# Kernel tuning notes

Measured on AMD Instinct MI355X. Metric: run time of the kernel, lower is better.

The kernel has to match this reference:

```python
import jax, jax.numpy as jnp
import numpy as np

D_MODEL = 768
NUM_HEADS = 12
D_K = D_MODEL // NUM_HEADS
BATCH = 1
SEQ = 4096


def setup_inputs() -> dict:
    key = jax.random.key(0)
    ks = jax.random.split(key, 11)
    s = 0.02
    inp = {
        'Q': jax.random.normal(ks[0], (BATCH, SEQ, D_MODEL), jnp.float32),
        'K': jax.random.normal(ks[1], (BATCH, SEQ, D_MODEL), jnp.float32),
        'V': jax.random.normal(ks[2], (BATCH, SEQ, D_MODEL), jnp.float32),
        'Wq': jax.random.normal(ks[3], (D_MODEL, D_MODEL), jnp.float32) * s,
        'bq': jnp.zeros((D_MODEL,), jnp.float32),
        'Wk': jax.random.normal(ks[4], (D_MODEL, D_MODEL), jnp.float32) * s,
        'bk': jnp.zeros((D_MODEL,), jnp.float32),
        'Wv': jax.random.normal(ks[5], (D_MODEL, D_MODEL), jnp.float32) * s,
        'bv': jnp.zeros((D_MODEL,), jnp.float32),
        'Wo': jax.random.normal(ks[6], (D_MODEL, D_MODEL), jnp.float32) * s,
        'bo': jnp.zeros((D_MODEL,), jnp.float32),
    }
    return inp


def reference(Q, K, V, Wq, bq, Wk, bk, Wv, bv, Wo, bo):
    B, S, _ = Q.shape
    # Linear projections (torch Linear: x @ W^T + b)
    q = Q @ Wq.T + bq
    k = K @ Wk.T + bk
    v = V @ Wv.T + bv
    # split heads: (B, S, D) -> (B, H, S, d_k)
    def split(x):
        return x.reshape(B, S, NUM_HEADS, D_K).transpose(0, 2, 1, 3)
    q, k, v = split(q), split(k), split(v)
    # scaled dot-product attention (dropout = identity in eval)
    scores = jnp.einsum('bhqd,bhkd->bhqk', q, k) / jnp.sqrt(jnp.float32(D_K))
    attn_weights = jax.nn.softmax(scores, axis=-1)
    ctx = jnp.einsum('bhqk,bhkd->bhqd', attn_weights, v)
    # merge heads and output projection
    ctx = ctx.transpose(0, 2, 1, 3).reshape(B, S, D_MODEL)
    output = ctx @ Wo.T + bo
    return (output, attn_weights)
```

## Files before the change

kernel.cpp:

```cpp
#include <hip/hip_runtime.h>
#include <hip/hip_bf16.h>

#define S 4096
#define DM 768
#define NH 12
#define DK 64
#define KSPLIT 2
#define KHALF (S / KSPLIT)
#define RPARTS 8
#define RCHUNK (S / RPARTS)

typedef __bf16 bf16x8 __attribute__((ext_vector_type(8)));
typedef __bf16 bf16x4 __attribute__((ext_vector_type(4)));
typedef float f32x4 __attribute__((ext_vector_type(4)));
using bf16 = __hip_bfloat16;

__device__ inline bf16x8 load_frag(const bf16* p) {
    return *reinterpret_cast<const bf16x8*>(p);
}

__global__ void k_detect(const unsigned int* __restrict__ q, int* __restrict__ flag) {
    const int lane = threadIdx.x;
    int cnt = 0;
    for (int i = lane; i < 1024; i += 64) {
        const unsigned int w = q[i];
        const int e = (w >> 7) & 0xFF;
        if (e >= 192 || (e > 0 && e < 64)) cnt++;
    }
    for (int m = 1; m < 64; m <<= 1) cnt += __shfl_xor(cnt, m, 64);
    if (lane == 0) flag[0] = (cnt > 64) ? 1 : 0;
}

__device__ inline void cast_body(const void* src, bf16* dst, int n, int isf32) {
    const int stride = gridDim.x * 256 * 8;
    for (int i = (blockIdx.x * 256 + threadIdx.x) * 8; i < n; i += stride) {
        if (isf32) {
            const float* s = (const float*)src + i;
            float4 a = *(const float4*)(s);
            float4 b = *(const float4*)(s + 4);
            bf16x8 o;
            o[0] = (__bf16)a.x; o[1] = (__bf16)a.y; o[2] = (__bf16)a.z; o[3] = (__bf16)a.w;
            o[4] = (__bf16)b.x; o[5] = (__bf16)b.y; o[6] = (__bf16)b.z; o[7] = (__bf16)b.w;
            *reinterpret_cast<bf16x8*>(dst + i) = o;
        } else {
            *reinterpret_cast<bf16x8*>(dst + i) =
                *reinterpret_cast<const bf16x8*>((const __bf16*)src + i);
        }
    }
}

__global__ __launch_bounds__(256) void k_cast3(
    const void* s0, const void* s1, const void* s2,
    bf16* d0, bf16* d1, bf16* d2, int n, const int* __restrict__ flag) {
    const int t = blockIdx.y;
    const void* s = (t == 0) ? s0 : (t == 1) ? s1 : s2;
    bf16* d = (t == 0) ? d0 : (t == 1) ? d1 : d2;
    cast_body(s, d, n, flag[0]);
}

__global__ __launch_bounds__(256) void k_cast4(
    const void* s0, const void* s1, const void* s2, const void* s3,
    bf16* d0, bf16* d1, bf16* d2, bf16* d3, int n, const int* __restrict__ flag) {
    const int t = blockIdx.y;
    const void* s = (t == 0) ? s0 : (t == 1) ? s1 : (t == 2) ? s2 : s3;
    bf16* d = (t == 0) ? d0 : (t == 1) ? d1 : (t == 2) ? d2 : d3;
    cast_body(s, d, n, flag[0]);
}

__device__ inline void proj_body(
    const bf16* __restrict__ X, const bf16* __restrict__ W,
    const bf16* __restrict__ bias, void* __restrict__ dstv, int mode, int isf32)
{
    const int lane = threadIdx.x & 63;
    const int w    = threadIdx.x >> 6;
    const int lr   = lane & 15, lg = lane >> 4;
    const int rbase = blockIdx.x * 64 + w * 16;
    const int nbase = blockIdx.y * 64;

    f32x4 acc[4] = {};
    const bf16* xrow = X + (size_t)(rbase + lr) * DM + lg * 8;
    for (int kk = 0; kk < DM; kk += 32) {
        bf16x8 a = load_frag(xrow + kk);
#pragma unroll
        for (int nt = 0; nt < 4; ++nt) {
            bf16x8 b = load_frag(W + (size_t)(nbase + nt * 16 + lr) * DM + kk + lg * 8);
            acc[nt] = __builtin_amdgcn_mfma_f32_16x16x32_bf16(a, b, acc[nt], 0, 0, 0);
        }
    }
#pragma unroll
    for (int nt = 0; nt < 4; ++nt) {
        const int col = nbase + nt * 16 + lr;
        const float bv = __bfloat162float(bias[col]);
#pragma unroll
        for (int r = 0; r < 4; ++r) {
            const int row = rbase + lg * 4 + r;
            const float v = acc[nt][r] + bv;
            size_t off;
            if (mode == 2) off = (size_t)col * S + row;
            else           off = (size_t)(col >> 6) * (S * DK) + (size_t)row * DK + (col & 63);
            ((bf16*)dstv)[off] = __float2bfloat16(v);
        }
    }
}

__global__ __launch_bounds__(256) void k_proj_qkv(
    const bf16* __restrict__ Qc, const bf16* __restrict__ Kc, const bf16* __restrict__ Vc,
    const bf16* __restrict__ Wq, const bf16* __restrict__ Wk, const bf16* __restrict__ Wv,
    const bf16* __restrict__ bq, const bf16* __restrict__ bk, const bf16* __restrict__ bv,
    bf16* __restrict__ qh, bf16* __restrict__ kh, bf16* __restrict__ vt,
    const int* __restrict__ flag)
{
    const int z = blockIdx.z;
    const bf16* X = (z == 0) ? Qc : (z == 1) ? Kc : Vc;
    const bf16* W = (z == 0) ? Wq : (z == 1) ? Wk : Wv;
    const bf16* B = (z == 0) ? bq : (z == 1) ? bk : bv;
    bf16* D      = (z == 0) ? qh : (z == 1) ? kh : vt;
    proj_body(X, W, B, D, (z == 2) ? 2 : 0, flag[0]);
}

__global__ __launch_bounds__(256) void k_proj_out(
    const bf16* __restrict__ ctxp, const bf16* __restrict__ W,
    const bf16* __restrict__ bias, void* __restrict__ dstv,
    const int* __restrict__ flag)
{
    const int isf32 = flag[0];
    const int lane = threadIdx.x & 63;
    const int w    = threadIdx.x >> 6;
    const int lr   = lane & 15, lg = lane >> 4;
    const int rbase = blockIdx.x * 64 + w * 16;
    const int nbase = blockIdx.y * 64;

    f32x4 acc[4] = {};
    const bf16* x0 = ctxp + (size_t)(rbase + lr) * DM + lg * 8;
    const bf16* x1 = x0 + (size_t)S * DM;
    for (int kk = 0; kk < DM; kk += 32) {
        bf16x8 a0 = load_frag(x0 + kk);
        bf16x8 a1 = load_frag(x1 + kk);
        bf16x8 a;
#pragma unroll
        for (int j = 0; j < 8; ++j)
            a[j] = (__bf16)((float)a0[j] + (float)a1[j]);
#pragma unroll
        for (int nt = 0; nt < 4; ++nt) {
            bf16x8 b = load_frag(W + (size_t)(nbase + nt * 16 + lr) * DM + kk + lg * 8);
            acc[nt] = __builtin_amdgcn_mfma_f32_16x16x32_bf16(a, b, acc[nt], 0, 0, 0);
        }
    }
#pragma unroll
    for (int nt = 0; nt < 4; ++nt) {
        const int col = nbase + nt * 16 + lr;
        const float bv = __bfloat162float(bias[col]);
#pragma unroll
        for (int r = 0; r < 4; ++r) {
            const int row = rbase + lg * 4 + r;
            const float v = acc[nt][r] + bv;
            const size_t off = (size_t)row * DM + col;
            if (isf32) ((float*)dstv)[off] = v;
            else       ((bf16*)dstv)[off] = __float2bfloat16(v);
        }
    }
}

__global__ __launch_bounds__(256) void k_rowsum(
    const bf16* __restrict__ qh, const bf16* __restrict__ kh,
    float* __restrict__ rs)
{
    const int lane = threadIdx.x & 63;
    const int w    = threadIdx.x >> 6;
    const int lr   = lane & 15;
    const int lg   = lane >> 4;
    const int h    = blockIdx.y;
    const int part = blockIdx.z;
    const int qw   = blockIdx.x * 256 + w * 64;

    const bf16* qb = qh + (size_t)h * (S * DK);
    const bf16* kb = kh + (size_t)h * (S * DK);
    bf16x8 aq[4][2];
#pragma unroll
    for (int qs = 0; qs < 4; ++qs) {
        aq[qs][0] = load_frag(qb + (size_t)(qw + qs * 16 + lr) * DK + lg * 8);
        aq[qs][1] = load_frag(qb + (size_t)(qw + qs * 16 + lr) * DK + 32 + lg * 8);
    }

    float s[4] = {0.f, 0.f, 0.f, 0.f};
    for (int kp = part * RCHUNK; kp < part * RCHUNK + RCHUNK; kp += 16) {
        bf16x8 b0 = load_frag(kb + (size_t)(kp + lr) * DK + lg * 8);
        bf16x8 b1 = load_frag(kb + (size_t)(kp + lr) * DK + 32 + lg * 8);
#pragma unroll
        for (int qs = 0; qs < 4; ++qs) {
            f32x4 d = {};
            d = __builtin_amdgcn_mfma_f32_16x16x32_bf16(b0, aq[qs][0], d, 0, 0, 0);
            d = __builtin_amdgcn_mfma_f32_16x16x32_bf16(b1, aq[qs][1], d, 0, 0, 0);
            s[qs] += __expf(d[0] * 0.125f) + __expf(d[1] * 0.125f) +
                     __expf(d[2] * 0.125f) + __expf(d[3] * 0.125f);
        }
    }
#pragma unroll
    for (int qs = 0; qs < 4; ++qs) {
        float v = s[qs];
        v += __shfl_xor(v, 16, 64);
        v += __shfl_xor(v, 32, 64);
        if (lg == 0)
            rs[((size_t)part * NH + h) * S + qw + qs * 16 + lr] = v;
    }
}

__global__ __launch_bounds__(256) void k_attn(
    const bf16* __restrict__ qh, const bf16* __restrict__ kh,
    const bf16* __restrict__ vt, const float* __restrict__ rs,
    void* __restrict__ doutv, bf16* __restrict__ ctxp,
    const int* __restrict__ flag)
{
    __shared__ __align__(16) bf16 Plds[4][2][16][136];
    const int isf32 = flag[0];
    const int lane = threadIdx.x & 63;
    const int w    = threadIdx.x >> 6;
    const int lr   = lane & 15, lg = lane >> 4;
    const int h    = blockIdx.y;
    const int half = blockIdx.z;
    const int q0w  = blockIdx.x * 128 + w * 32;
    const int k0   = half * KHALF;

    const bf16* qb = qh + (size_t)h * (S * DK);
    const bf16* kb = kh + (size_t)h * (S * DK);
    const bf16* vb = vt + (size_t)h * (S * DK);

    bf16x8 aq[2][2];
    float  inv[2];
#pragma unroll
    for (int qs = 0; qs < 2; ++qs) {
        const int qr = q0w + qs * 16 + lr;
        aq[qs][0] = load_frag(qb + (size_t)qr * DK + lg * 8);
        aq[qs][1] = load_frag(qb + (size_t)qr * DK + 32 + lg * 8);
        float ssum = 0.f;
#pragma unroll
        for (int p = 0; p < RPARTS; ++p)
            ssum += rs[((size_t)p * NH + h) * S + qr];
        inv[qs] = 1.0f / ssum;
    }

    float* poutF = (float*)doutv + (size_t)S * DM + (size_t)h * S * S;
    bf16*  poutB = (bf16*)doutv  + (size_t)S * DM + (size_t)h * S * S;

    const int fr2 = lane >> 5;
    const int fc2 = (lane & 31) * 4;

    f32x4 acc[2][4] = {};
    for (int tp = 0; tp < KHALF / 128; ++tp) {
#pragma unroll
        for (int tt = 0; tt < 2; ++tt) {
            const int kt = k0 + tp * 128 + tt * 64;
            const int cb = tt * 64;
            bf16x8 vv[4][2];
#pragma unroll
            for (int dt = 0; dt < 4; ++dt) {
                vv[dt][0] = load_frag(vb + (size_t)(dt * 16 + lr) * S + kt + lg * 8);
                vv[dt][1] = load_frag(vb + (size_t)(dt * 16 + lr) * S + kt + 32 + lg * 8);
            }
#pragma unroll
            for (int sub = 0; sub < 4; ++sub) {
                const int kp = kt + sub * 16;
                bf16x8 b0 = load_frag(kb + (size_t)(kp + lr) * DK + lg * 8);
                bf16x8 b1 = load_frag(kb + (size_t)(kp + lr) * DK + 32 + lg * 8);
#pragma unroll
                for (int qs = 0; qs < 2; ++qs) {
                    f32x4 d = {};
                    d = __builtin_amdgcn_mfma_f32_16x16x32_bf16(b0, aq[qs][0], d, 0, 0, 0);
                    d = __builtin_amdgcn_mfma_f32_16x16x32_bf16(b1, aq[qs][1], d, 0, 0, 0);
                    bf16x4 pv;
                    pv[0] = (__bf16)(__expf(d[0] * 0.125f) * inv[qs]);
                    pv[1] = (__bf16)(__expf(d[1] * 0.125f) * inv[qs]);
                    pv[2] = (__bf16)(__expf(d[2] * 0.125f) * inv[qs]);
                    pv[3] = (__bf16)(__expf(d[3] * 0.125f) * inv[qs]);
                    *reinterpret_cast<bf16x4*>(
                        &Plds[w][qs][lr][cb + sub * 16 + 4 * lg]) = pv;
                }
            }
            bf16x8 ap[2][2];
#pragma unroll
            for (int qs = 0; qs < 2; ++qs) {
                ap[qs][0] = *reinterpret_cast<const bf16x8*>(&Plds[w][qs][lr][cb + lg * 8]);
                ap[qs][1] = *reinterpret_cast<const bf16x8*>(&Plds[w][qs][lr][cb + 32 + lg * 8]);
            }
#pragma unroll
            for (int dt = 0; dt < 4; ++dt) {
#pragma unroll
                for (int qs = 0; qs < 2; ++qs) {
                    acc[qs][dt] = __builtin_amdgcn_mfma_f32_16x16x32_bf16(ap[qs][0], vv[dt][0], acc[qs][dt], 0, 0, 0);
                    acc[qs][dt] = __builtin_amdgcn_mfma_f32_16x16x32_bf16(ap[qs][1], vv[dt][1], acc[qs][dt], 0, 0, 0);
                }
            }
        }
        const int ktbase = k0 + tp * 128;
        if (isf32) {
#pragma unroll
            for (int j = 0; j < 16; ++j) {
                const int row = 2 * j + fr2;
                const int qs = row >> 4, rr = row & 15;
                bf16x4 x = *reinterpret_cast<const bf16x4*>(&Plds[w][qs][rr][fc2]);
                f32x4 o;
                o[0] = (float)x[0]; o[1] = (float)x[1];
                o[2] = (float)x[2]; o[3] = (float)x[3];
                __builtin_nontemporal_store(
                    o, reinterpret_cast<f32x4*>(
                           poutF + (size_t)(q0w + row) * S + ktbase + fc2));
            }
        } else {
#pragma unroll
            for (int j = 0; j < 16; ++j) {
                const int row = 2 * j + fr2;
                const int qs = row >> 4, rr = row & 15;
                bf16x4 x = *reinterpret_cast<const bf16x4*>(&Plds[w][qs][rr][fc2]);
                *reinterpret_cast<bf16x4*>(
                    poutB + (size_t)(q0w + row) * S + ktbase + fc2) = x;
            }
        }
    }
    bf16* cp = ctxp + (size_t)half * S * DM;
#pragma unroll
    for (int qs = 0; qs < 2; ++qs)
#pragma unroll
        for (int dt = 0; dt < 4; ++dt)
#pragma unroll
            for (int r = 0; r < 4; ++r)
                cp[(size_t)(q0w + qs * 16 + 4 * lg + r) * DM + h * DK + dt * 16 + lr] =
                    __float2bfloat16(acc[qs][dt][r]);
}

extern "C" void kernel_launch(void* const* d_in, const int* in_sizes, int n_in,
                              void* d_out, int out_size, void* d_ws, size_t ws_size,
                              hipStream_t stream) {
    char* wsb = (char*)d_ws;
    int*   flag = (int*)wsb;
    float* rs   = (float*)(wsb + 16);
    bf16*  conv = (bf16*)(wsb + 16 + (size_t)RPARTS * NH * S * 4);

    const size_t nQ = (size_t)S * DM, nW = (size_t)DM * DM, nB = DM;
    bf16* Qc  = conv;
    bf16* Kc  = Qc + nQ;
    bf16* Vc  = Kc + nQ;
    bf16* Wqc = Vc + nQ;
    bf16* Wkc = Wqc + nW;
    bf16* Wvc = Wkc + nW;
    bf16* Woc = Wvc + nW;
    bf16* bqc = Woc + nW;
    bf16* bkc = bqc + nB;
    bf16* bvc = bkc + nB;
    bf16* boc = bvc + nB;
    bf16* qh  = boc + nB;
    bf16* kh  = qh + nQ;
    bf16* vt  = kh + nQ;
    bf16* ctxp = Qc;

    const size_t need = (size_t)((char*)(vt + nQ) - wsb);
    if (ws_size < need) return;

    dim3 blk(256);
    k_detect<<<1, 64, 0, stream>>>((const unsigned int*)d_in[0], flag);

    k_cast3<<<dim3((int)(nQ / 2048), 3), blk, 0, stream>>>(
        d_in[0], d_in[1], d_in[2], Qc, Kc, Vc, (int)nQ, flag);
    k_cast4<<<dim3((int)(nW / 2048), 4), blk, 0, stream>>>(
        d_in[3], d_in[5], d_in[7], d_in[9], Wqc, Wkc, Wvc, Woc, (int)nW, flag);
    k_cast4<<<dim3(1, 4), blk, 0, stream>>>(
        d_in[4], d_in[6], d_in[8], d_in[10], bqc, bkc, bvc, boc, (int)nB, flag);

    k_proj_qkv<<<dim3(S / 64, DM / 64, 3), blk, 0, stream>>>(
        Qc, Kc, Vc, Wqc, Wkc, Wvc, bqc, bkc, bvc, qh, kh, vt, flag);
    k_rowsum<<<dim3(S / 256, NH, RPARTS), blk, 0, stream>>>(qh, kh, rs);
    k_attn<<<dim3(S / 128, NH, KSPLIT), blk, 0, stream>>>(qh, kh, vt, rs, d_out, ctxp, flag);
    k_proj_out<<<dim3(S / 64, DM / 64), blk, 0, stream>>>(ctxp, Woc, boc, d_out, flag);
}
```

Baseline: 470.4 us.

## Double-buffer K/V register tiles in attention kernel and fold normalization into exp

The attention kernel now prefetches the next 64-key K and V fragments into a second register set while the current tile's QK^T, softmax and PV MFMAs run, so global load latency overlaps with compute. The softmax normalization becomes exp(x*0.125 - log(sum)) through a single FMA instead of a multiply after the exp. Launch bounds now request 2 blocks per CU. The extra register buffers raise register pressure and the occupancy hint may cause spills. On the last iteration the prefetch reloads the same tile, which is redundant but harmless.

Measured after the change: 468.5 us. No clear change (-0.4%).

```diff
diff --git a/kernel.cpp b/kernel.cpp
--- a/kernel.cpp
+++ b/kernel.cpp
@@ -205,7 +205,59 @@
     }
 }
 
-__global__ __launch_bounds__(256) void k_attn(
+__device__ inline void load_ktile(const bf16* kb, int kt, int lr, int lg,
+                                  bf16x8 dst[4][2]) {
+#pragma unroll
+    for (int sub = 0; sub < 4; ++sub) {
+        dst[sub][0] = load_frag(kb + (size_t)(kt + sub * 16 + lr) * DK + lg * 8);
+        dst[sub][1] = load_frag(kb + (size_t)(kt + sub * 16 + lr) * DK + 32 + lg * 8);
+    }
+}
+__device__ inline void load_vtile(const bf16* vb, int kt, int lr, int lg,
+                                  bf16x8 dst[4][2]) {
+#pragma unroll
+    for (int dt = 0; dt < 4; ++dt) {
+        dst[dt][0] = load_frag(vb + (size_t)(dt * 16 + lr) * S + kt + lg * 8);
+        dst[dt][1] = load_frag(vb + (size_t)(dt * 16 + lr) * S + kt + 32 + lg * 8);
+    }
+}
+__device__ inline void qk_tile(const bf16x8 kc[4][2], const bf16x8 aq[2][2],
+                               const float linv[2], bf16 Pw[2][16][136],
+                               int cb, int lr, int lg) {
+#pragma unroll
+    for (int sub = 0; sub < 4; ++sub) {
+#pragma unroll
+        for (int qs = 0; qs < 2; ++qs) {
+            f32x4 d = {};
+            d = __builtin_amdgcn_mfma_f32_16x16x32_bf16(kc[sub][0], aq[qs][0], d, 0, 0, 0);
+            d = __builtin_amdgcn_mfma_f32_16x16x32_bf16(kc[sub][1], aq[qs][1], d, 0, 0, 0);
+            bf16x4 pv;
+            pv[0] = (__bf16)__expf(__builtin_fmaf(d[0], 0.125f, linv[qs]));
+            pv[1] = (__bf16)__expf(__builtin_fmaf(d[1], 0.125f, linv[qs]));
+            pv[2] = (__bf16)__expf(__builtin_fmaf(d[2], 0.125f, linv[qs]));
+            pv[3] = (__bf16)__expf(__builtin_fmaf(d[3], 0.125f, linv[qs]));
+            *reinterpret_cast<bf16x4*>(&Pw[qs][lr][cb + sub * 16 + 4 * lg]) = pv;
+        }
+    }
+}
+__device__ inline void pv_tile(const bf16x8 vc[4][2], const bf16 Pw[2][16][136],
+                               f32x4 acc[2][4], int cb, int lr, int lg) {
+    bf16x8 ap[2][2];
+#pragma unroll
+    for (int qs = 0; qs < 2; ++qs) {
+        ap[qs][0] = *reinterpret_cast<const bf16x8*>(&Pw[qs][lr][cb + lg * 8]);
+        ap[qs][1] = *reinterpret_cast<const bf16x8*>(&Pw[qs][lr][cb + 32 + lg * 8]);
+    }
+#pragma unroll
+    for (int dt = 0; dt < 4; ++dt)
+#pragma unroll
+        for (int qs = 0; qs < 2; ++qs) {
+            acc[qs][dt] = __builtin_amdgcn_mfma_f32_16x16x32_bf16(ap[qs][0], vc[dt][0], acc[qs][dt], 0, 0, 0);
+            acc[qs][dt] = __builtin_amdgcn_mfma_f32_16x16x32_bf16(ap[qs][1], vc[dt][1], acc[qs][dt], 0, 0, 0);
+        }
+}
+
+__global__ __launch_bounds__(256, 2) void k_attn(
     const bf16* __restrict__ qh, const bf16* __restrict__ kh,
     const bf16* __restrict__ vt, const float* __restrict__ rs,
     void* __restrict__ doutv, bf16* __restrict__ ctxp,
@@ -220,13 +272,14 @@
     const int half = blockIdx.z;
     const int q0w  = blockIdx.x * 128 + w * 32;
     const int k0   = half * KHALF;
+    const int NT   = KHALF / 64;
 
     const bf16* qb = qh + (size_t)h * (S * DK);
     const bf16* kb = kh + (size_t)h * (S * DK);
     const bf16* vb = vt + (size_t)h * (S * DK);
 
     bf16x8 aq[2][2];
-    float  inv[2];
+    float  linv[2];
 #pragma unroll
     for (int qs = 0; qs < 2; ++qs) {
         const int qr = q0w + qs * 16 + lr;
@@ -236,62 +289,31 @@
 #pragma unroll
         for (int p = 0; p < RPARTS; ++p)
             ssum += rs[((size_t)p * NH + h) * S + qr];
-        inv[qs] = 1.0f / ssum;
+        linv[qs] = -__logf(ssum);
     }
 
     float* poutF = (float*)doutv + (size_t)S * DM + (size_t)h * S * S;
     bf16*  poutB = (bf16*)doutv  + (size_t)S * DM + (size_t)h * S * S;
-
     const int fr2 = lane >> 5;
     const int fc2 = (lane & 31) * 4;
 
+    bf16x8 kA[4][2], vA[4][2], kB[4][2], vB[4][2];
+    load_ktile(kb, k0, lr, lg, kA);
+    load_vtile(vb, k0, lr, lg, vA);
+
     f32x4 acc[2][4] = {};
-    for (int tp = 0; tp < KHALF / 128; ++tp) {
-#pragma unroll
-        for (int tt = 0; tt < 2; ++tt) {
-            const int kt = k0 + tp * 128 + tt * 64;
-            const int cb = tt * 64;
-            bf16x8 vv[4][2];
-#pragma unroll
-            for (int dt = 0; dt < 4; ++dt) {
-                vv[dt][0] = load_frag(vb + (size_t)(dt * 16 + lr) * S + kt + lg * 8);
-                vv[dt][1] = load_frag(vb + (size_t)(dt * 16 + lr) * S + kt + 32 + lg * 8);
-            }
-#pragma unroll
-            for (int sub = 0; sub < 4; ++sub) {
-                const int kp = kt + sub * 16;
-                bf16x8 b0 = load_frag(kb + (size_t)(kp + lr) * DK + lg * 8);
-                bf16x8 b1 = load_frag(kb + (size_t)(kp + lr) * DK + 32 + lg * 8);
-#pragma unroll
-                for (int qs = 0; qs < 2; ++qs) {
-                    f32x4 d = {};
-                    d = __builtin_amdgcn_mfma_f32_16x16x32_bf16(b0, aq[qs][0], d, 0, 0, 0);
-                    d = __builtin_amdgcn_mfma_f32_16x16x32_bf16(b1, aq[qs][1], d, 0, 0, 0);
-                    bf16x4 pv;
-                    pv[0] = (__bf16)(__expf(d[0] * 0.125f) * inv[qs]);
-                    pv[1] = (__bf16)(__expf(d[1] * 0.125f) * inv[qs]);
-                    pv[2] = (__bf16)(__expf(d[2] * 0.125f) * inv[qs]);
-                    pv[3] = (__bf16)(__expf(d[3] * 0.125f) * inv[qs]);
-                    *reinterpret_cast<bf16x4*>(
-                        &Plds[w][qs][lr][cb + sub * 16 + 4 * lg]) = pv;
-                }
-            }
-            bf16x8 ap[2][2];
-#pragma unroll
-            for (int qs = 0; qs < 2; ++qs) {
-                ap[qs][0] = *reinterpret_cast<const bf16x8*>(&Plds[w][qs][lr][cb + lg * 8]);
-                ap[qs][1] = *reinterpret_cast<const bf16x8*>(&Plds[w][qs][lr][cb + 32 + lg * 8]);
-            }
-#pragma unroll
-            for (int dt = 0; dt < 4; ++dt) {
-#pragma unroll
-                for (int qs = 0; qs < 2; ++qs) {
-                    acc[qs][dt] = __builtin_amdgcn_mfma_f32_16x16x32_bf16(ap[qs][0], vv[dt][0], acc[qs][dt], 0, 0, 0);
-                    acc[qs][dt] = __builtin_amdgcn_mfma_f32_16x16x32_bf16(ap[qs][1], vv[dt][1], acc[qs][dt], 0, 0, 0);
-                }
-            }
-        }
-        const int ktbase = k0 + tp * 128;
+    for (int p = 0; p < NT / 2; ++p) {
+        const int ktA  = k0 + 2 * p * 64;
+        const int ktB  = ktA + 64;
+        const int ktA2 = (2 * p + 2 < NT) ? ktB + 64 : ktB;
+        load_ktile(kb, ktB, lr, lg, kB);
+        load_vtile(vb, ktB, lr, lg, vB);
+        qk_tile(kA, aq, linv, Plds[w], 0, lr, lg);
+        pv_tile(vA, Plds[w], acc, 0, lr, lg);
+        load_ktile(kb, ktA2, lr, lg, kA);
+        load_vtile(vb, ktA2, lr, lg, vA);
+        qk_tile(kB, aq, linv, Plds[w], 64, lr, lg);
+        pv_tile(vB, Plds[w], acc, 64, lr, lg);
         if (isf32) {
 #pragma unroll
             for (int j = 0; j < 16; ++j) {
@@ -303,7 +325,7 @@
                 o[2] = (float)x[2]; o[3] = (float)x[3];
                 __builtin_nontemporal_store(
                     o, reinterpret_cast<f32x4*>(
-                           poutF + (size_t)(q0w + row) * S + ktbase + fc2));
+                           poutF + (size_t)(q0w + row) * S + ktA + fc2));
             }
         } else {
 #pragma unroll
@@ -312,7 +334,7 @@
                 const int qs = row >> 4, rr = row & 15;
                 bf16x4 x = *reinterpret_cast<const bf16x4*>(&Plds[w][qs][rr][fc2]);
                 *reinterpret_cast<bf16x4*>(
-                    poutB + (size_t)(q0w + row) * S + ktbase + fc2) = x;
+                    poutB + (size_t)(q0w + row) * S + ktA + fc2) = x;
             }
         }
     }
```

## Drop key split in attention, merge cast kernels, fold normalization into exp

Applied to the files above, without the earlier changes.

The attention kernel no longer splits the key range in two. Each 128-thread block now covers 64 queries over all keys in 256-key groups, so the output projection reads a single context buffer instead of summing two partials. The three cast launches are merged into one kernel driven by an argument struct. The softmax normalization is folded into the exponent as an added log term, which removes a multiply. The cost is fewer, longer-running attention blocks (the same 768 blocks but half as many waves), which may lower latency hiding.

New measurement: 464.7 us. Within noise of the previous version (-1.2%).

```diff
diff --git a/kernel.cpp b/kernel.cpp
--- a/kernel.cpp
+++ b/kernel.cpp
@@ -5,8 +5,6 @@
 #define DM 768
 #define NH 12
 #define DK 64
-#define KSPLIT 2
-#define KHALF (S / KSPLIT)
 #define RPARTS 8
 #define RCHUNK (S / RPARTS)
 
@@ -31,40 +29,33 @@
     if (lane == 0) flag[0] = (cnt > 64) ? 1 : 0;
 }
 
-__device__ inline void cast_body(const void* src, bf16* dst, int n, int isf32) {
+struct CastArgs {
+    const void* s[11];
+    bf16* d[11];
+    int n[11];
+};
+
+__global__ __launch_bounds__(256) void k_cast_all(CastArgs a, const int* __restrict__ flag) {
+    const int t = blockIdx.y;
+    const void* src = a.s[t];
+    bf16* dst = a.d[t];
+    const int n = a.n[t];
+    const int isf32 = flag[0];
     const int stride = gridDim.x * 256 * 8;
     for (int i = (blockIdx.x * 256 + threadIdx.x) * 8; i < n; i += stride) {
         if (isf32) {
             const float* s = (const float*)src + i;
-            float4 a = *(const float4*)(s);
-            float4 b = *(const float4*)(s + 4);
+            float4 x = *(const float4*)(s);
+            float4 y = *(const float4*)(s + 4);
             bf16x8 o;
-            o[0] = (__bf16)a.x; o[1] = (__bf16)a.y; o[2] = (__bf16)a.z; o[3] = (__bf16)a.w;
-            o[4] = (__bf16)b.x; o[5] = (__bf16)b.y; o[6] = (__bf16)b.z; o[7] = (__bf16)b.w;
+            o[0] = (__bf16)x.x; o[1] = (__bf16)x.y; o[2] = (__bf16)x.z; o[3] = (__bf16)x.w;
+            o[4] = (__bf16)y.x; o[5] = (__bf16)y.y; o[6] = (__bf16)y.z; o[7] = (__bf16)y.w;
             *reinterpret_cast<bf16x8*>(dst + i) = o;
         } else {
             *reinterpret_cast<bf16x8*>(dst + i) =
                 *reinterpret_cast<const bf16x8*>((const __bf16*)src + i);
         }
     }
-}
-
-__global__ __launch_bounds__(256) void k_cast3(
-    const void* s0, const void* s1, const void* s2,
-    bf16* d0, bf16* d1, bf16* d2, int n, const int* __restrict__ flag) {
-    const int t = blockIdx.y;
-    const void* s = (t == 0) ? s0 : (t == 1) ? s1 : s2;
-    bf16* d = (t == 0) ? d0 : (t == 1) ? d1 : d2;
-    cast_body(s, d, n, flag[0]);
-}
-
-__global__ __launch_bounds__(256) void k_cast4(
-    const void* s0, const void* s1, const void* s2, const void* s3,
-    bf16* d0, bf16* d1, bf16* d2, bf16* d3, int n, const int* __restrict__ flag) {
-    const int t = blockIdx.y;
-    const void* s = (t == 0) ? s0 : (t == 1) ? s1 : (t == 2) ? s2 : s3;
-    bf16* d = (t == 0) ? d0 : (t == 1) ? d1 : (t == 2) ? d2 : d3;
-    cast_body(s, d, n, flag[0]);
 }
 
 __device__ inline void proj_body(
@@ -119,7 +110,7 @@
 }
 
 __global__ __launch_bounds__(256) void k_proj_out(
-    const bf16* __restrict__ ctxp, const bf16* __restrict__ W,
+    const bf16* __restrict__ ctx, const bf16* __restrict__ W,
     const bf16* __restrict__ bias, void* __restrict__ dstv,
     const int* __restrict__ flag)
 {
@@ -131,15 +122,9 @@
     const int nbase = blockIdx.y * 64;
 
     f32x4 acc[4] = {};
-    const bf16* x0 = ctxp + (size_t)(rbase + lr) * DM + lg * 8;
-    const bf16* x1 = x0 + (size_t)S * DM;
+    const bf16* xrow = ctx + (size_t)(rbase + lr) * DM + lg * 8;
     for (int kk = 0; kk < DM; kk += 32) {
-        bf16x8 a0 = load_frag(x0 + kk);
-        bf16x8 a1 = load_frag(x1 + kk);
-        bf16x8 a;
-#pragma unroll
-        for (int j = 0; j < 8; ++j)
-            a[j] = (__bf16)((float)a0[j] + (float)a1[j]);
+        bf16x8 a = load_frag(xrow + kk);
 #pragma unroll
         for (int nt = 0; nt < 4; ++nt) {
             bf16x8 b = load_frag(W + (size_t)(nbase + nt * 16 + lr) * DM + kk + lg * 8);
@@ -205,28 +190,26 @@
     }
 }
 
-__global__ __launch_bounds__(256) void k_attn(
+__global__ __launch_bounds__(128) void k_attn(
     const bf16* __restrict__ qh, const bf16* __restrict__ kh,
     const bf16* __restrict__ vt, const float* __restrict__ rs,
-    void* __restrict__ doutv, bf16* __restrict__ ctxp,
+    void* __restrict__ doutv, bf16* __restrict__ ctx,
     const int* __restrict__ flag)
 {
-    __shared__ __align__(16) bf16 Plds[4][2][16][136];
+    __shared__ __align__(16) bf16 Plds[2][2][16][264];
     const int isf32 = flag[0];
     const int lane = threadIdx.x & 63;
     const int w    = threadIdx.x >> 6;
     const int lr   = lane & 15, lg = lane >> 4;
     const int h    = blockIdx.y;
-    const int half = blockIdx.z;
-    const int q0w  = blockIdx.x * 128 + w * 32;
-    const int k0   = half * KHALF;
+    const int q0w  = blockIdx.x * 64 + w * 32;
 
     const bf16* qb = qh + (size_t)h * (S * DK);
     const bf16* kb = kh + (size_t)h * (S * DK);
     const bf16* vb = vt + (size_t)h * (S * DK);
 
     bf16x8 aq[2][2];
-    float  inv[2];
+    float  linv[2];
 #pragma unroll
     for (int qs = 0; qs < 2; ++qs) {
         const int qr = q0w + qs * 16 + lr;
@@ -236,20 +219,17 @@
 #pragma unroll
         for (int p = 0; p < RPARTS; ++p)
             ssum += rs[((size_t)p * NH + h) * S + qr];
-        inv[qs] = 1.0f / ssum;
+        linv[qs] = -__logf(ssum);
     }
 
     float* poutF = (float*)doutv + (size_t)S * DM + (size_t)h * S * S;
     bf16*  poutB = (bf16*)doutv  + (size_t)S * DM + (size_t)h * S * S;
 
-    const int fr2 = lane >> 5;
-    const int fc2 = (lane & 31) * 4;
-
     f32x4 acc[2][4] = {};
-    for (int tp = 0; tp < KHALF / 128; ++tp) {
-#pragma unroll
-        for (int tt = 0; tt < 2; ++tt) {
-            const int kt = k0 + tp * 128 + tt * 64;
+    for (int g = 0; g < S / 256; ++g) {
+#pragma unroll
+        for (int tt = 0; tt < 4; ++tt) {
+            const int kt = g * 256 + tt * 64;
             const int cb = tt * 64;
             bf16x8 vv[4][2];
 #pragma unroll
@@ -268,10 +248,10 @@
                     d = __builtin_amdgcn_mfma_f32_16x16x32_bf16(b0, aq[qs][0], d, 0, 0, 0);
                     d = __builtin_amdgcn_mfma_f32_16x16x32_bf16(b1, aq[qs][1], d, 0, 0, 0);
                     bf16x4 pv;
-                    pv[0] = (__bf16)(__expf(d[0] * 0.125f) * inv[qs]);
-                    pv[1] = (__bf16)(__expf(d[1] * 0.125f) * inv[qs]);
-                    pv[2] = (__bf16)(__expf(d[2] * 0.125f) * inv[qs]);
-                    pv[3] = (__bf16)(__expf(d[3] * 0.125f) * inv[qs]);
+                    pv[0] = (__bf16)__expf(__builtin_fmaf(d[0], 0.125f, linv[qs]));
+                    pv[1] = (__bf16)__expf(__builtin_fmaf(d[1], 0.125f, linv[qs]));
+                    pv[2] = (__bf16)__expf(__builtin_fmaf(d[2], 0.125f, linv[qs]));
+                    pv[3] = (__bf16)__expf(__builtin_fmaf(d[3], 0.125f, linv[qs]));
                     *reinterpret_cast<bf16x4*>(
                         &Plds[w][qs][lr][cb + sub * 16 + 4 * lg]) = pv;
                 }
@@ -291,39 +271,36 @@
                 }
             }
         }
-        const int ktbase = k0 + tp * 128;
+        const int ktbase = g * 256;
         if (isf32) {
 #pragma unroll
-            for (int j = 0; j < 16; ++j) {
-                const int row = 2 * j + fr2;
-                const int qs = row >> 4, rr = row & 15;
-                bf16x4 x = *reinterpret_cast<const bf16x4*>(&Plds[w][qs][rr][fc2]);
+            for (int j = 0; j < 32; ++j) {
+                const int qs = j >> 4, rr = j & 15;
+                bf16x4 x = *reinterpret_cast<const bf16x4*>(&Plds[w][qs][rr][lane * 4]);
                 f32x4 o;
                 o[0] = (float)x[0]; o[1] = (float)x[1];
                 o[2] = (float)x[2]; o[3] = (float)x[3];
                 __builtin_nontemporal_store(
                     o, reinterpret_cast<f32x4*>(
-                           poutF + (size_t)(q0w + row) * S + ktbase + fc2));
+                           poutF + (size_t)(q0w + j) * S + ktbase + lane * 4));
             }
         } else {
 #pragma unroll
-            for (int j = 0; j < 16; ++j) {
-                const int row = 2 * j + fr2;
-                const int qs = row >> 4, rr = row & 15;
-                bf16x4 x = *reinterpret_cast<const bf16x4*>(&Plds[w][qs][rr][fc2]);
+            for (int j = 0; j < 32; ++j) {
+                const int qs = j >> 4, rr = j & 15;
+                bf16x4 x = *reinterpret_cast<const bf16x4*>(&Plds[w][qs][rr][lane * 4]);
                 *reinterpret_cast<bf16x4*>(
-                    poutB + (size_t)(q0w + row) * S + ktbase + fc2) = x;
-            }
-        }
-    }
-    bf16* cp = ctxp + (size_t)half * S * DM;
+                    poutB + (size_t)(q0w + j) * S + ktbase + lane * 4) = x;
+            }
+        }
+    }
 #pragma unroll
     for (int qs = 0; qs < 2; ++qs)
 #pragma unroll
         for (int dt = 0; dt < 4; ++dt)
 #pragma unroll
             for (int r = 0; r < 4; ++r)
-                cp[(size_t)(q0w + qs * 16 + 4 * lg + r) * DM + h * DK + dt * 16 + lr] =
+                ctx[(size_t)(q0w + qs * 16 + 4 * lg + r) * DM + h * DK + dt * 16 + lr] =
                     __float2bfloat16(acc[qs][dt][r]);
 }
 
@@ -350,7 +327,7 @@
     bf16* qh  = boc + nB;
     bf16* kh  = qh + nQ;
     bf16* vt  = kh + nQ;
-    bf16* ctxp = Qc;
+    bf16* ctx = Qc;
 
     const size_t need = (size_t)((char*)(vt + nQ) - wsb);
     if (ws_size < need) return;
@@ -358,16 +335,23 @@
     dim3 blk(256);
     k_detect<<<1, 64, 0, stream>>>((const unsigned int*)d_in[0], flag);
 
-    k_cast3<<<dim3((int)(nQ / 2048), 3), blk, 0, stream>>>(
-        d_in[0], d_in[1], d_in[2], Qc, Kc, Vc, (int)nQ, flag);
-    k_cast4<<<dim3((int)(nW / 2048), 4), blk, 0, stream>>>(
-        d_in[3], d_in[5], d_in[7], d_in[9], Wqc, Wkc, Wvc, Woc, (int)nW, flag);
-    k_cast4<<<dim3(1, 4), blk, 0, stream>>>(
-        d_in[4], d_in[6], d_in[8], d_in[10], bqc, bkc, bvc, boc, (int)nB, flag);
+    CastArgs ca;
+    ca.s[0] = d_in[0];  ca.d[0] = Qc;   ca.n[0] = (int)nQ;
+    ca.s[1] = d_in[1];  ca.d[1] = Kc;   ca.n[1] = (int)nQ;
+    ca.s[2] = d_in[2];  ca.d[2] = Vc;   ca.n[2] = (int)nQ;
+    ca.s[3] = d_in[3];  ca.d[3] = Wqc;  ca.n[3] = (int)nW;
+    ca.s[4] = d_in[5];  ca.d[4] = Wkc;  ca.n[4] = (int)nW;
+    ca.s[5] = d_in[7];  ca.d[5] = Wvc;  ca.n[5] = (int)nW;
+    ca.s[6] = d_in[9];  ca.d[6] = Woc;  ca.n[6] = (int)nW;
+    ca.s[7] = d_in[4];  ca.d[7] = bqc;  ca.n[7] = (int)nB;
+    ca.s[8] = d_in[6];  ca.d[8] = bkc;  ca.n[8] = (int)nB;
+    ca.s[9] = d_in[8];  ca.d[9] = bvc;  ca.n[9] = (int)nB;
+    ca.s[10] = d_in[10]; ca.d[10] = boc; ca.n[10] = (int)nB;
+    k_cast_all<<<dim3(512, 11), blk, 0, stream>>>(ca, flag);
 
     k_proj_qkv<<<dim3(S / 64, DM / 64, 3), blk, 0, stream>>>(
         Qc, Kc, Vc, Wqc, Wkc, Wvc, bqc, bkc, bvc, qh, kh, vt, flag);
     k_rowsum<<<dim3(S / 256, NH, RPARTS), blk, 0, stream>>>(qh, kh, rs);
-    k_attn<<<dim3(S / 128, NH, KSPLIT), blk, 0, stream>>>(qh, kh, vt, rs, d_out, ctxp, flag);
-    k_proj_out<<<dim3(S / 64, DM / 64), blk, 0, stream>>>(ctxp, Woc, boc, d_out, flag);
-}
+    k_attn<<<dim3(S / 64, NH), dim3(128), 0, stream>>>(qh, kh, vt, rs, d_out, ctx, flag);
+    k_proj_out<<<dim3(S / 64, DM / 64), blk, 0, stream>>>(ctx, Woc, boc, d_out, flag);
+}
```
